# Kernel optimization log

Hardware: AMD Instinct MI355X
Metric: run time of the kernel (lower is better)

Reference implementation:

```python
import jax, jax.numpy as jnp
import numpy as np

N = 100000
E = 1600000
D_IN = 128
D_H = 128
N_LAYERS = 3


def setup_inputs() -> dict:
    key = jax.random.key(0)
    ks = jax.random.split(key, 4 + 3 * N_LAYERS)
    x = jax.random.normal(ks[0], (N, D_IN), dtype=jnp.float32)
    edge_index = jax.random.randint(ks[1], (2, E), 0, N, dtype=jnp.int64)
    inp = {"x": x, "edge_index": edge_index}
    d_prev = D_IN
    for i in range(N_LAYERS):
        s = 1.0 / np.sqrt(d_prev)
        inp[f"w_rel{i}"] = jax.random.normal(ks[2 + 3 * i], (D_H, d_prev), dtype=jnp.float32) * s
        inp[f"b_rel{i}"] = jnp.zeros((D_H,), dtype=jnp.float32)
        inp[f"w_root{i}"] = jax.random.normal(ks[3 + 3 * i], (D_H, d_prev), dtype=jnp.float32) * s
        d_prev = D_H
    inp["w_out"] = jax.random.normal(ks[-2], (1, D_H), dtype=jnp.float32) / np.sqrt(D_H)
    inp["b_out"] = jnp.zeros((1,), dtype=jnp.float32)
    return inp


def _graph_conv(x, src, dst, w_rel, b_rel, w_root):
    # PyG GraphConv: out_i = W_rel @ sum_{j->i} x_j + b_rel + W_root @ x_i
    msg = x[src]                                        # [E, d] gather
    aggr = jax.ops.segment_sum(msg, dst, num_segments=N)  # [N, d] scatter-add
    return aggr @ w_rel.T + b_rel + x @ w_root.T


def reference(x, edge_index, w_rel0, b_rel0, w_root0, w_rel1, b_rel1, w_root1,
              w_rel2, b_rel2, w_root2, w_out, b_out):
    src, dst = edge_index[0], edge_index[1]
    params = [(w_rel0, b_rel0, w_root0), (w_rel1, b_rel1, w_root1), (w_rel2, b_rel2, w_root2)]
    h = x
    for w_rel, b_rel, w_root in params:
        h = jax.nn.relu(_graph_conv(h, src, dst, w_rel, b_rel, w_root))
    return h @ w_out.T + b_out  # [N, 1]
```

## Files before the change

### kernel.cpp

```cpp
#include <hip/hip_runtime.h>

constexpr int N_NODES = 100000;
constexpr int N_EDGES = 1600000;
constexpr int CAP = 64;
constexpr int NPB = 128;
constexpr int NBIN = (N_NODES + NPB - 1) / NPB;
constexpr int NGRP = 32;
constexpr int SEGCAP = 128;
constexpr int NBLK_A = 1024;
constexpr int EPB = (N_EDGES + NBLK_A - 1) / NBLK_A;
constexpr int CONV_BLKS = (N_NODES * 64) / 256;
constexpr int GCNT_BLKS = (NBIN * NGRP + 255) / 256;

typedef short short8 __attribute__((ext_vector_type(8)));
typedef float f32x4 __attribute__((ext_vector_type(4)));

__device__ __forceinline__ unsigned short f2bf(float f) {
    unsigned int u = __float_as_uint(f);
    unsigned int r = (u + 0x7fff + ((u >> 16) & 1)) >> 16;
    return (unsigned short)r;
}
__device__ __forceinline__ float bflo(unsigned int u) { return __uint_as_float(u << 16); }
__device__ __forceinline__ float bfhi(unsigned int u) { return __uint_as_float(u & 0xffff0000u); }


__global__ __launch_bounds__(256) void prep(const float* __restrict__ x,
                                            unsigned short* __restrict__ A,
                                            const float* __restrict__ wrel0,
                                            const float* __restrict__ wroot0,
                                            const float* __restrict__ wrel1,
                                            const float* __restrict__ wroot1,
                                            const float* __restrict__ wrel2,
                                            const float* __restrict__ wroot2,
                                            unsigned short* __restrict__ pW,
                                            int* __restrict__ gcnt) {
    int b = blockIdx.x;
    if (b < CONV_BLKS) {
        int i = b * 256 + threadIdx.x;
        int node = i >> 6, c2 = (i & 63) * 2;
        float2 v = *(const float2*)&x[(size_t)node * 128 + c2];
        unsigned int out = (unsigned int)f2bf(v.x) | ((unsigned int)f2bf(v.y) << 16);
        *(unsigned int*)&A[(size_t)node * 256 + 128 + c2] = out;
    } else if (b < CONV_BLKS + 384) {
        int bb = b - CONV_BLKS;
        int layer = bb >> 7;
        int t = (bb & 127) * 256 + threadIdx.x;
        const float* wrel  = (layer == 0) ? wrel0  : (layer == 1) ? wrel1  : wrel2;
        const float* wroot = (layer == 0) ? wroot0 : (layer == 1) ? wroot1 : wroot2;
        int j = t & 7, lane = (t >> 3) & 63, ks = (t >> 9) & 7, nt = (t >> 12) & 7;
        int k = ks * 32 + ((lane >> 4) << 3) + j;
        int n = nt * 16 + (lane & 15);
        float v = (k < 128) ? wrel[n * 128 + k] : wroot[n * 128 + (k - 128)];
        pW[(size_t)layer * 32768 + t] = f2bf(v);
    } else {
        int idx = (b - CONV_BLKS - 384) * 256 + threadIdx.x;
        if (idx < NBIN * NGRP) gcnt[idx] = 0;
    }
}

__global__ __launch_bounds__(256) void partition_pairs(const int* __restrict__ src,
                                                       const int* __restrict__ dst,
                                                       int* __restrict__ gcnt,
                                                       int* __restrict__ pairs) {
    __shared__ int hist[NBIN];
    __shared__ int bl[NBIN];
    for (int j = threadIdx.x; j < NBIN; j += 256) hist[j] = 0;
    __syncthreads();
    int base = blockIdx.x * EPB;
    int grp = blockIdx.x >> 5;
    int pv[7], pr[7], pb[7];
    bool val[7];
    #pragma unroll
    for (int k = 0; k < 7; ++k) {
        int off = k * 256 + threadIdx.x;
        int e = base + off;
        val[k] = (off < EPB) && (e < N_EDGES);
        pv[k] = pr[k] = pb[k] = 0;
        if (val[k]) {
            int d = __builtin_nontemporal_load(dst + e);
            int s = __builtin_nontemporal_load(src + e);
            pb[k] = d >> 7;
            pv[k] = ((d & 127) << 17) | s;
            pr[k] = atomicAdd(&hist[pb[k]], 1);
        }
    }
    __syncthreads();
    for (int j = threadIdx.x; j < NBIN; j += 256) {
        int h = hist[j];
        bl[j] = h ? atomicAdd(&gcnt[j * NGRP + grp], h) : 0;
    }
    __syncthreads();
    #pragma unroll
    for (int k = 0; k < 7; ++k)
        if (val[k]) {
            int idx = bl[pb[k]] + pr[k];
            if (idx < SEGCAP)
                pairs[((size_t)pb[k] * NGRP + grp) * SEGCAP + idx] = pv[k];
        }
}

__global__ __launch_bounds__(256) void bucket_build(const int* __restrict__ gcnt,
                                                    const int* __restrict__ pairs,
                                                    int* __restrict__ cnt,
                                                    int* __restrict__ bkt) {
    __shared__ int cnt_l[NPB];
    __shared__ int bkt_l[NPB * CAP];
    int j = blockIdx.x;
    for (int t = threadIdx.x; t < NPB; t += 256) cnt_l[t] = 0;
    __syncthreads();
    int wave = threadIdx.x >> 6, lane = threadIdx.x & 63;
    for (int g = wave; g < NGRP; g += 4) {
        int n = gcnt[j * NGRP + g];
        n = (n > SEGCAP) ? SEGCAP : n;
        const int* seg = pairs + ((size_t)j * NGRP + g) * SEGCAP;
        for (int k = lane; k < n; k += 64) {
            int p = __builtin_nontemporal_load(seg + k);
            int dl = p >> 17;
            int s = p & 0x1FFFF;
            int pos = atomicAdd(&cnt_l[dl], 1);
            if (pos < CAP) bkt_l[(dl << 6) + pos] = s;
        }
    }
    __syncthreads();
    int base_node = j * NPB;
    for (int idx = threadIdx.x; idx < NPB * 16; idx += 256) {
        int node = base_node + (idx >> 4);
        if (node < N_NODES)
            ((uint4*)bkt)[(size_t)node * 16 + (idx & 15)] = ((const uint4*)bkt_l)[idx];
    }
    for (int t = threadIdx.x; t < NPB; t += 256) {
        int node = base_node + t;
        if (node < N_NODES) cnt[node] = cnt_l[t];
    }
}

__global__ __launch_bounds__(256) void gather_bucket(const int* __restrict__ cnt_arr,
                                                     const int* __restrict__ bkt,
                                                     unsigned short* __restrict__ A) {
    int wid = (blockIdx.x * 256 + threadIdx.x) >> 6;
    int lane = threadIdx.x & 63;
    if (wid >= N_NODES) return;
    int cnt = __builtin_nontemporal_load(cnt_arr + wid);
    cnt = (cnt > CAP) ? CAP : cnt;
    int myidx = __builtin_nontemporal_load(bkt + (wid << 6) + lane);
    int g = lane >> 4;
    int ch = lane & 15;
    float acc[8] = {};
    int e = 0;
    for (; e + 16 <= cnt; e += 16) {
        int s0 = __shfl(myidx, e + g);
        int s1 = __shfl(myidx, e + 4 + g);
        int s2 = __shfl(myidx, e + 8 + g);
        int s3 = __shfl(myidx, e + 12 + g);
        uint4 u0 = *(const uint4*)&A[(size_t)s0 * 256 + 128 + ch * 8];
        uint4 u1 = *(const uint4*)&A[(size_t)s1 * 256 + 128 + ch * 8];
        uint4 u2 = *(const uint4*)&A[(size_t)s2 * 256 + 128 + ch * 8];
        uint4 u3 = *(const uint4*)&A[(size_t)s3 * 256 + 128 + ch * 8];
        acc[0] += bflo(u0.x) + bflo(u1.x) + bflo(u2.x) + bflo(u3.x);
        acc[1] += bfhi(u0.x) + bfhi(u1.x) + bfhi(u2.x) + bfhi(u3.x);
        acc[2] += bflo(u0.y) + bflo(u1.y) + bflo(u2.y) + bflo(u3.y);
        acc[3] += bfhi(u0.y) + bfhi(u1.y) + bfhi(u2.y) + bfhi(u3.y);
        acc[4] += bflo(u0.z) + bflo(u1.z) + bflo(u2.z) + bflo(u3.z);
        acc[5] += bfhi(u0.z) + bfhi(u1.z) + bfhi(u2.z) + bfhi(u3.z);
        acc[6] += bflo(u0.w) + bflo(u1.w) + bflo(u2.w) + bflo(u3.w);
        acc[7] += bfhi(u0.w) + bfhi(u1.w) + bfhi(u2.w) + bfhi(u3.w);
    }
    for (; e + 8 <= cnt; e += 8) {
        int s0 = __shfl(myidx, e + g);
        int s1 = __shfl(myidx, e + 4 + g);
        uint4 u0 = *(const uint4*)&A[(size_t)s0 * 256 + 128 + ch * 8];
        uint4 u1 = *(const uint4*)&A[(size_t)s1 * 256 + 128 + ch * 8];
        acc[0] += bflo(u0.x) + bflo(u1.x);
        acc[1] += bfhi(u0.x) + bfhi(u1.x);
        acc[2] += bflo(u0.y) + bflo(u1.y);
        acc[3] += bfhi(u0.y) + bfhi(u1.y);
        acc[4] += bflo(u0.z) + bflo(u1.z);
        acc[5] += bfhi(u0.z) + bfhi(u1.z);
        acc[6] += bflo(u0.w) + bflo(u1.w);
        acc[7] += bfhi(u0.w) + bfhi(u1.w);
    }
    for (; e < cnt; e += 4) {
        int ei = e + g;
        int s0 = __shfl(myidx, ei & 63);
        if (ei < cnt) {
            uint4 u0 = *(const uint4*)&A[(size_t)s0 * 256 + 128 + ch * 8];
            acc[0] += bflo(u0.x); acc[1] += bfhi(u0.x);
            acc[2] += bflo(u0.y); acc[3] += bfhi(u0.y);
            acc[4] += bflo(u0.z); acc[5] += bfhi(u0.z);
            acc[6] += bflo(u0.w); acc[7] += bfhi(u0.w);
        }
    }
    #pragma unroll
    for (int j = 0; j < 8; ++j) {
        acc[j] += __shfl_xor(acc[j], 16);
        acc[j] += __shfl_xor(acc[j], 32);
    }
    if (g == 0) {
        uint4 o;
        o.x = (unsigned int)f2bf(acc[0]) | ((unsigned int)f2bf(acc[1]) << 16);
        o.y = (unsigned int)f2bf(acc[2]) | ((unsigned int)f2bf(acc[3]) << 16);
        o.z = (unsigned int)f2bf(acc[4]) | ((unsigned int)f2bf(acc[5]) << 16);
        o.w = (unsigned int)f2bf(acc[6]) | ((unsigned int)f2bf(acc[7]) << 16);
        *(uint4*)&A[(size_t)wid * 256 + ch * 8] = o;
    }
}

template <bool LAST>
__global__ __launch_bounds__(256, 3) void mfma_transform(unsigned short* __restrict__ A,
                                                         const unsigned short* __restrict__ packedW,
                                                         const float* __restrict__ brel,
                                                         const float* __restrict__ w_out,
                                                         const float* __restrict__ b_out,
                                                         float* __restrict__ outF) {
    __shared__ unsigned short sW[16384];
    int wave = threadIdx.x >> 6, lane = threadIdx.x & 63;
    int l15 = lane & 15, lhi = lane >> 4;
    int brow = blockIdx.x * 256 + wave * 64;
    float bias[8], wo[8];
    #pragma unroll
    for (int nt = 0; nt < 8; ++nt) {
        bias[nt] = brel[nt * 16 + l15];
        if (LAST) wo[nt] = w_out[nt * 16 + l15];
    }
    float bout = LAST ? b_out[0] : 0.f;

    for (int rtp = 0; rtp < 2; ++rtp) {
        int r0 = brow + rtp * 32;
        short8 a[2][8];
        #pragma unroll
        for (int rt = 0; rt < 2; ++rt) {
            int row = r0 + rt * 16 + l15;
            if (row >= N_NODES) row = N_NODES - 1;
            const unsigned short* ap = &A[(size_t)row * 256 + lhi * 8];
            #pragma unroll
            for (int ks = 0; ks < 8; ++ks) a[rt][ks] = *(const short8*)(ap + ks * 32);
        }
        float pacc[2][4];
        #pragma unroll
        for (int rt = 0; rt < 2; ++rt)
            #pragma unroll
            for (int rg = 0; rg < 4; ++rg) pacc[rt][rg] = 0.f;

        for (int half = 0; half < 2; ++half) {
            __syncthreads();
            {
                const uint4* gsrc = (const uint4*)(packedW + (size_t)half * 16384);
                uint4* s = (uint4*)sW;
                for (int i = threadIdx.x; i < 2048; i += 256) s[i] = gsrc[i];
            }
            __syncthreads();
            f32x4 acc[2][4] = {};
            #pragma unroll
            for (int ntl = 0; ntl < 4; ++ntl) {
                #pragma unroll
                for (int ks = 0; ks < 8; ++ks) {
                    short8 b = *(const short8*)&sW[(size_t)((ntl * 8 + ks) * 64 + lane) * 8];
                    acc[0][ntl] = __builtin_amdgcn_mfma_f32_16x16x32_bf16(a[0][ks], b, acc[0][ntl], 0, 0, 0);
                    acc[1][ntl] = __builtin_amdgcn_mfma_f32_16x16x32_bf16(a[1][ks], b, acc[1][ntl], 0, 0, 0);
                }
            }
            #pragma unroll
            for (int rt = 0; rt < 2; ++rt) {
                #pragma unroll
                for (int ntl = 0; ntl < 4; ++ntl) {
                    int nt = half * 4 + ntl;
                    #pragma unroll
                    for (int rg = 0; rg < 4; ++rg) {
                        float v = fmaxf(acc[rt][ntl][rg] + bias[nt], 0.f);
                        if (LAST) {
                            pacc[rt][rg] += v * wo[nt];
                        } else {
                            int row = r0 + rt * 16 + lhi * 4 + rg;
                            if (row < N_NODES)
                                A[(size_t)row * 256 + 128 + nt * 16 + l15] = f2bf(v);
                        }
                    }
                }
            }
        }
        if (LAST) {
            #pragma unroll
            for (int rt = 0; rt < 2; ++rt) {
                #pragma unroll
                for (int rg = 0; rg < 4; ++rg) {
                    float p = pacc[rt][rg];
                    p += __shfl_xor(p, 1);
                    p += __shfl_xor(p, 2);
                    p += __shfl_xor(p, 4);
                    p += __shfl_xor(p, 8);
                    int row = r0 + rt * 16 + lhi * 4 + rg;
                    if (l15 == 0 && row < N_NODES) outF[row] = p + bout;
                }
            }
        }
    }
}

extern "C" void kernel_launch(void* const* d_in, const int* in_sizes, int n_in,
                              void* d_out, int out_size, void* d_ws, size_t ws_size,
                              hipStream_t stream) {
    const float* x      = (const float*)d_in[0];
    const int*   edge   = (const int*)d_in[1];
    const int*   src    = edge;
    const int*   dst    = edge + N_EDGES;
    const float* w_rel[3]  = {(const float*)d_in[2], (const float*)d_in[5], (const float*)d_in[8]};
    const float* b_rel[3]  = {(const float*)d_in[3], (const float*)d_in[6], (const float*)d_in[9]};
    const float* w_root[3] = {(const float*)d_in[4], (const float*)d_in[7], (const float*)d_in[10]};
    const float* w_out  = (const float*)d_in[11];
    const float* b_out  = (const float*)d_in[12];

    unsigned short* A  = (unsigned short*)d_ws;
    unsigned short* pW = A + (size_t)N_NODES * 256;
    int* cnt   = (int*)(pW + 3 * 32768);
    int* bkt   = cnt + N_NODES;
    int* gcnt  = bkt + (size_t)N_NODES * CAP;
    int* pairs = gcnt + NBIN * NGRP;

    prep<<<CONV_BLKS + 384 + GCNT_BLKS, 256, 0, stream>>>(x, A, w_rel[0], w_root[0],
                                                          w_rel[1], w_root[1],
                                                          w_rel[2], w_root[2], pW, gcnt);

    partition_pairs<<<NBLK_A, 256, 0, stream>>>(src, dst, gcnt, pairs);
    bucket_build<<<NBIN, 256, 0, stream>>>(gcnt, pairs, cnt, bkt);

    const int gblocks = (N_NODES * 64 + 255) / 256;
    const int xblocks = (N_NODES + 255) / 256;

    gather_bucket<<<gblocks, 256, 0, stream>>>(cnt, bkt, A);
    mfma_transform<false><<<xblocks, 256, 0, stream>>>(A, pW + 0 * 32768, b_rel[0],
                                                       nullptr, nullptr, nullptr);
    gather_bucket<<<gblocks, 256, 0, stream>>>(cnt, bkt, A);
    mfma_transform<false><<<xblocks, 256, 0, stream>>>(A, pW + 1 * 32768, b_rel[1],
                                                       nullptr, nullptr, nullptr);
    gather_bucket<<<gblocks, 256, 0, stream>>>(cnt, bkt, A);
    mfma_transform<true><<<xblocks, 256, 0, stream>>>(A, pW + 2 * 32768, b_rel[2],
                                                      w_out, b_out, (float*)d_out);
}
```

Before: 324.8 us.

## Fuse edge partitioning into prep kernel and pack bf16 accumulation as float2

The edge partition pass moves into the prep kernel as extra blocks, and the gcnt zeroing moves to a hipMemsetAsync placed before it. This removes one kernel launch and lets partitioning overlap with the feature conversion and weight packing. In gather_bucket the bf16 unpack and accumulate now uses float2 vectors, which may let the compiler emit packed FP32 adds. In exchange, every prep block now reserves the large shared histogram arrays, which can lower occupancy for the conversion blocks, and a memset call is added.

```diff
diff --git a/kernel.cpp b/kernel.cpp
--- a/kernel.cpp
+++ b/kernel.cpp
@@ -10,10 +10,10 @@
 constexpr int NBLK_A = 1024;
 constexpr int EPB = (N_EDGES + NBLK_A - 1) / NBLK_A;
 constexpr int CONV_BLKS = (N_NODES * 64) / 256;
-constexpr int GCNT_BLKS = (NBIN * NGRP + 255) / 256;
 
 typedef short short8 __attribute__((ext_vector_type(8)));
 typedef float f32x4 __attribute__((ext_vector_type(4)));
+typedef float f32x2 __attribute__((ext_vector_type(2)));
 
 __device__ __forceinline__ unsigned short f2bf(float f) {
     unsigned int u = __float_as_uint(f);
@@ -22,6 +22,12 @@
 }
 __device__ __forceinline__ float bflo(unsigned int u) { return __uint_as_float(u << 16); }
 __device__ __forceinline__ float bfhi(unsigned int u) { return __uint_as_float(u & 0xffff0000u); }
+__device__ __forceinline__ f32x2 unpk(unsigned int u) {
+    f32x2 v;
+    v.x = __uint_as_float(u << 16);
+    v.y = __uint_as_float(u & 0xffff0000u);
+    return v;
+}
 
 
 __global__ __launch_bounds__(256) void prep(const float* __restrict__ x,
@@ -33,7 +39,10 @@
                                             const float* __restrict__ wrel2,
                                             const float* __restrict__ wroot2,
                                             unsigned short* __restrict__ pW,
-                                            int* __restrict__ gcnt) {
+                                            const int* __restrict__ src,
+                                            const int* __restrict__ dst,
+                                            int* __restrict__ gcnt,
+                                            int* __restrict__ pairs) {
     int b = blockIdx.x;
     if (b < CONV_BLKS) {
         int i = b * 256 + threadIdx.x;
@@ -53,50 +62,43 @@
         float v = (k < 128) ? wrel[n * 128 + k] : wroot[n * 128 + (k - 128)];
         pW[(size_t)layer * 32768 + t] = f2bf(v);
     } else {
-        int idx = (b - CONV_BLKS - 384) * 256 + threadIdx.x;
-        if (idx < NBIN * NGRP) gcnt[idx] = 0;
-    }
-}
-
-__global__ __launch_bounds__(256) void partition_pairs(const int* __restrict__ src,
-                                                       const int* __restrict__ dst,
-                                                       int* __restrict__ gcnt,
-                                                       int* __restrict__ pairs) {
-    __shared__ int hist[NBIN];
-    __shared__ int bl[NBIN];
-    for (int j = threadIdx.x; j < NBIN; j += 256) hist[j] = 0;
-    __syncthreads();
-    int base = blockIdx.x * EPB;
-    int grp = blockIdx.x >> 5;
-    int pv[7], pr[7], pb[7];
-    bool val[7];
-    #pragma unroll
-    for (int k = 0; k < 7; ++k) {
-        int off = k * 256 + threadIdx.x;
-        int e = base + off;
-        val[k] = (off < EPB) && (e < N_EDGES);
-        pv[k] = pr[k] = pb[k] = 0;
-        if (val[k]) {
-            int d = __builtin_nontemporal_load(dst + e);
-            int s = __builtin_nontemporal_load(src + e);
-            pb[k] = d >> 7;
-            pv[k] = ((d & 127) << 17) | s;
-            pr[k] = atomicAdd(&hist[pb[k]], 1);
-        }
-    }
-    __syncthreads();
-    for (int j = threadIdx.x; j < NBIN; j += 256) {
-        int h = hist[j];
-        bl[j] = h ? atomicAdd(&gcnt[j * NGRP + grp], h) : 0;
-    }
-    __syncthreads();
-    #pragma unroll
-    for (int k = 0; k < 7; ++k)
-        if (val[k]) {
-            int idx = bl[pb[k]] + pr[k];
-            if (idx < SEGCAP)
-                pairs[((size_t)pb[k] * NGRP + grp) * SEGCAP + idx] = pv[k];
-        }
+        __shared__ int hist[NBIN];
+        __shared__ int bl[NBIN];
+        int bb2 = b - CONV_BLKS - 384;
+        for (int j = threadIdx.x; j < NBIN; j += 256) hist[j] = 0;
+        __syncthreads();
+        int base = bb2 * EPB;
+        int grp = bb2 >> 5;
+        int pv[7], pr[7], pb[7];
+        bool val[7];
+        #pragma unroll
+        for (int k = 0; k < 7; ++k) {
+            int off = k * 256 + threadIdx.x;
+            int e = base + off;
+            val[k] = (off < EPB) && (e < N_EDGES);
+            pv[k] = pr[k] = pb[k] = 0;
+            if (val[k]) {
+                int d = __builtin_nontemporal_load(dst + e);
+                int s = __builtin_nontemporal_load(src + e);
+                pb[k] = d >> 7;
+                pv[k] = ((d & 127) << 17) | s;
+                pr[k] = atomicAdd(&hist[pb[k]], 1);
+            }
+        }
+        __syncthreads();
+        for (int j = threadIdx.x; j < NBIN; j += 256) {
+            int h = hist[j];
+            bl[j] = h ? atomicAdd(&gcnt[j * NGRP + grp], h) : 0;
+        }
+        __syncthreads();
+        #pragma unroll
+        for (int k = 0; k < 7; ++k)
+            if (val[k]) {
+                int idx = bl[pb[k]] + pr[k];
+                if (idx < SEGCAP)
+                    pairs[((size_t)pb[k] * NGRP + grp) * SEGCAP + idx] = pv[k];
+            }
+    }
 }
 
 __global__ __launch_bounds__(256) void bucket_build(const int* __restrict__ gcnt,
@@ -145,7 +147,7 @@
     int myidx = __builtin_nontemporal_load(bkt + (wid << 6) + lane);
     int g = lane >> 4;
     int ch = lane & 15;
-    float acc[8] = {};
+    f32x2 acc2[4] = {};
     int e = 0;
     for (; e + 16 <= cnt; e += 16) {
         int s0 = __shfl(myidx, e + g);
@@ -156,39 +158,37 @@
         uint4 u1 = *(const uint4*)&A[(size_t)s1 * 256 + 128 + ch * 8];
         uint4 u2 = *(const uint4*)&A[(size_t)s2 * 256 + 128 + ch * 8];
         uint4 u3 = *(const uint4*)&A[(size_t)s3 * 256 + 128 + ch * 8];
-        acc[0] += bflo(u0.x) + bflo(u1.x) + bflo(u2.x) + bflo(u3.x);
-        acc[1] += bfhi(u0.x) + bfhi(u1.x) + bfhi(u2.x) + bfhi(u3.x);
-        acc[2] += bflo(u0.y) + bflo(u1.y) + bflo(u2.y) + bflo(u3.y);
-        acc[3] += bfhi(u0.y) + bfhi(u1.y) + bfhi(u2.y) + bfhi(u3.y);
-        acc[4] += bflo(u0.z) + bflo(u1.z) + bflo(u2.z) + bflo(u3.z);
-        acc[5] += bfhi(u0.z) + bfhi(u1.z) + bfhi(u2.z) + bfhi(u3.z);
-        acc[6] += bflo(u0.w) + bflo(u1.w) + bflo(u2.w) + bflo(u3.w);
-        acc[7] += bfhi(u0.w) + bfhi(u1.w) + bfhi(u2.w) + bfhi(u3.w);
+        acc2[0] += unpk(u0.x) + unpk(u1.x) + unpk(u2.x) + unpk(u3.x);
+        acc2[1] += unpk(u0.y) + unpk(u1.y) + unpk(u2.y) + unpk(u3.y);
+        acc2[2] += unpk(u0.z) + unpk(u1.z) + unpk(u2.z) + unpk(u3.z);
+        acc2[3] += unpk(u0.w) + unpk(u1.w) + unpk(u2.w) + unpk(u3.w);
     }
     for (; e + 8 <= cnt; e += 8) {
         int s0 = __shfl(myidx, e + g);
         int s1 = __shfl(myidx, e + 4 + g);
         uint4 u0 = *(const uint4*)&A[(size_t)s0 * 256 + 128 + ch * 8];
         uint4 u1 = *(const uint4*)&A[(size_t)s1 * 256 + 128 + ch * 8];
-        acc[0] += bflo(u0.x) + bflo(u1.x);
-        acc[1] += bfhi(u0.x) + bfhi(u1.x);
-        acc[2] += bflo(u0.y) + bflo(u1.y);
-        acc[3] += bfhi(u0.y) + bfhi(u1.y);
-        acc[4] += bflo(u0.z) + bflo(u1.z);
-        acc[5] += bfhi(u0.z) + bfhi(u1.z);
-        acc[6] += bflo(u0.w) + bflo(u1.w);
-        acc[7] += bfhi(u0.w) + bfhi(u1.w);
+        acc2[0] += unpk(u0.x) + unpk(u1.x);
+        acc2[1] += unpk(u0.y) + unpk(u1.y);
+        acc2[2] += unpk(u0.z) + unpk(u1.z);
+        acc2[3] += unpk(u0.w) + unpk(u1.w);
     }
     for (; e < cnt; e += 4) {
         int ei = e + g;
         int s0 = __shfl(myidx, ei & 63);
         if (ei < cnt) {
             uint4 u0 = *(const uint4*)&A[(size_t)s0 * 256 + 128 + ch * 8];
-            acc[0] += bflo(u0.x); acc[1] += bfhi(u0.x);
-            acc[2] += bflo(u0.y); acc[3] += bfhi(u0.y);
-            acc[4] += bflo(u0.z); acc[5] += bfhi(u0.z);
-            acc[6] += bflo(u0.w); acc[7] += bfhi(u0.w);
-        }
+            acc2[0] += unpk(u0.x);
+            acc2[1] += unpk(u0.y);
+            acc2[2] += unpk(u0.z);
+            acc2[3] += unpk(u0.w);
+        }
+    }
+    float acc[8];
+    #pragma unroll
+    for (int j = 0; j < 4; ++j) {
+        acc[2 * j] = acc2[j].x;
+        acc[2 * j + 1] = acc2[j].y;
     }
     #pragma unroll
     for (int j = 0; j < 8; ++j) {
@@ -316,11 +316,11 @@
     int* gcnt  = bkt + (size_t)N_NODES * CAP;
     int* pairs = gcnt + NBIN * NGRP;
 
-    prep<<<CONV_BLKS + 384 + GCNT_BLKS, 256, 0, stream>>>(x, A, w_rel[0], w_root[0],
-                                                          w_rel[1], w_root[1],
-                                                          w_rel[2], w_root[2], pW, gcnt);
-
-    partition_pairs<<<NBLK_A, 256, 0, stream>>>(src, dst, gcnt, pairs);
+    hipMemsetAsync(gcnt, 0, NBIN * NGRP * sizeof(int), stream);
+    prep<<<CONV_BLKS + 384 + NBLK_A, 256, 0, stream>>>(x, A, w_rel[0], w_root[0],
+                                                       w_rel[1], w_root[1],
+                                                       w_rel[2], w_root[2], pW,
+                                                       src, dst, gcnt, pairs);
     bucket_build<<<NBIN, 256, 0, stream>>>(gcnt, pairs, cnt, bkt);
 
     const int gblocks = (N_NODES * 64 + 255) / 256;
```

Result: no change. 326.7 us (+0.6%).
